# Optimization experiments

Hardware: AMD Instinct MI355X
Metric: run time of the kernel (lower is better)

Reference implementation:

```python
import jax, jax.numpy as jnp
import numpy as np

N_FFT = 256
WINDOW_OUT = 64
N_BINS = N_FFT // 2 + 1  # 129


def _irfft_matrices(n_fft, window_out):
    n = n_fft // 2 + 1
    m_real = np.fft.irfft(np.eye(n), n=n_fft)          # [n, n_fft]
    m_imag = np.fft.irfft(1j * np.eye(n), n=n_fft)     # [n, n_fft]
    m_real = m_real[:, -window_out:]                   # truncate to last window_out samples
    m_imag = m_imag[:, -window_out:]
    return (jnp.asarray(m_real, dtype=jnp.float32), jnp.asarray(m_imag, dtype=jnp.float32))


def setup_inputs() -> dict:
    key = jax.random.key(0)
    k1, k2 = jax.random.split(key)
    re = jax.random.normal(k1, (64, 4000, N_BINS), dtype=jnp.float32)
    im = jax.random.normal(k2, (64, 4000, N_BINS), dtype=jnp.float32)
    m_real, m_imag = _irfft_matrices(N_FFT, WINDOW_OUT)
    return {"re": re, "im": im, "m_real": m_real, "m_imag": m_imag}


def reference(re, im, m_real, m_imag):
    # Dense IRFFT: out = re @ M_real + im @ M_imag, fused add of the two matmul outputs.
    # re, im: [B, T, n_bins]; m_real, m_imag: [n_bins, window_out] -> out: [B, T, window_out]
    return jnp.einsum('btn,no->bto', re, m_real) + jnp.einsum('btn,no->bto', im, m_imag)
```

## Files before the change

kernel.cpp:

```cpp
#include <hip/hip_runtime.h>
#include <hip/hip_bf16.h>

typedef __bf16 bf8 __attribute__((ext_vector_type(8)));
typedef float f32x4 __attribute__((ext_vector_type(4)));

#define NBINS 129
#define ROWS_IT 16
#define ITERS 16
#define MATB 8192
#define TAILB 512
#define BUFB (2 * MATB + TAILB)

__device__ __forceinline__ void gload_lds16(const float* src, char* ldsdst) {
    __builtin_amdgcn_global_load_lds(
        (const __attribute__((address_space(1))) void*)src,
        (__attribute__((address_space(3))) void*)ldsdst, 16, 0, 0);
}

__global__ __launch_bounds__(256, 3)
void irfft_mm(const float* __restrict__ re,
              const float* __restrict__ im,
              const float* __restrict__ mr,
              const float* __restrict__ mi,
              float* __restrict__ out)
{
    __shared__ __align__(16) char lds[3][BUFB];

    const int tid  = threadIdx.x;
    const int lane = tid & 63;
    const int w    = tid >> 6;
    const int r16  = lane & 15;
    const int q    = lane >> 4;
    const int rk   = r16 & 7;

    const long blockrow = (long)blockIdx.x * (ROWS_IT * ITERS);

    const int    smat  = w >> 1;
    const int    srow0 = (w & 1) * 8;
    const float* ssrc  = smat ? im : re;
    const int    lrow  = lane >> 5;
    const int    p     = lane & 31;

    #define STAGE(bn, rbn)                                                        \
        {                                                                         \
            char* _b = (bn);                                                      \
            const long _r = (rbn);                                                \
            _Pragma("unroll")                                                     \
            for (int i = 0; i < 4; ++i) {                                         \
                const int trow = srow0 + 2 * i + lrow;                            \
                const int g    = p ^ (trow & 7);   \
                gload_lds16(ssrc + (_r + trow) * (long)NBINS + g * 4,             \
                            _b + smat * MATB + (srow0 + 2 * i) * 512 + lane * 16);\
            }                                                                     \
            if (lane < 8)      \
                gload_lds16(ssrc + (_r + srow0 + lane) * (long)NBINS + 128,       \
                            _b + 2 * MATB + smat * 256 + (srow0 + lane) * 16);    \
        }

    STAGE(lds[0], blockrow);
    STAGE(lds[1], blockrow + ROWS_IT);

    bf8 afr[2][4];
    #pragma unroll
    for (int m = 0; m < 2; ++m) {
        const float* M = m ? mi : mr;
        #pragma unroll
        for (int t = 0; t < 4; ++t) {
            bf8 a;
            #pragma unroll
            for (int j = 0; j < 8; ++j)
                a[j] = (__bf16)M[(t * 32 + q * 8 + j) * 64 + w * 16 + r16];
            afr[m][t] = a;
        }
    }
    const f32x4 mt0 = *(const f32x4*)(mr + 128 * 64 + w * 16 + q * 4);
    const f32x4 mt1 = *(const f32x4*)(mi + 128 * 64 + w * 16 + q * 4);

    #pragma unroll
    for (int it = 0; it < ITERS; ++it) {
        char* bufc = lds[it % 3];
        const long rowbase = blockrow + it * ROWS_IT;

        __builtin_amdgcn_sched_barrier(0);
        if (it < ITERS - 1) asm volatile("s_waitcnt vmcnt(5)" ::: "memory");
        else                asm volatile("s_waitcnt vmcnt(0)" ::: "memory");
        __builtin_amdgcn_s_barrier();
        __builtin_amdgcn_sched_barrier(0);

        if (it + 2 < ITERS)
            STAGE(lds[(it + 2) % 3], rowbase + 2 * ROWS_IT);

        f32x4 acc = {0.0f, 0.0f, 0.0f, 0.0f};
        #pragma unroll
        for (int m = 0; m < 2; ++m) {
            const char* mb = bufc + m * MATB + r16 * 512;
            #pragma unroll
            for (int t = 0; t < 4; ++t) {
                const int j0 = t * 8 + q * 2;
                const f32x4 lo = *(const f32x4*)(mb + ((j0)     ^ rk) * 16);
                const f32x4 hi = *(const f32x4*)(mb + ((j0 + 1) ^ rk) * 16);
                bf8 bfr;
                #pragma unroll
                for (int jj = 0; jj < 4; ++jj) {
                    bfr[jj]     = (__bf16)lo[jj];
                    bfr[4 + jj] = (__bf16)hi[jj];
                }
                acc = __builtin_amdgcn_mfma_f32_16x16x32_bf16(afr[m][t], bfr, acc, 0, 0, 0);
            }
            const float xt = *(const float*)(bufc + 2 * MATB + m * 256 + r16 * 16);
            const f32x4 mt = m ? mt1 : mt0;
            #pragma unroll
            for (int jj = 0; jj < 4; ++jj) acc[jj] += xt * mt[jj];
        }

        *(f32x4*)(out + (rowbase + r16) * 64 + w * 16 + q * 4) = acc;
    }
    #undef STAGE
}

extern "C" void kernel_launch(void* const* d_in, const int* in_sizes, int n_in,
                              void* d_out, int out_size, void* d_ws, size_t ws_size,
                              hipStream_t stream)
{
    const float* re = (const float*)d_in[0];
    const float* im = (const float*)d_in[1];
    const float* mr = (const float*)d_in[2];
    const float* mi = (const float*)d_in[3];
    float* out = (float*)d_out;

    const long rows = (long)in_sizes[0] / NBINS;
    const int grid = (int)(rows / (ROWS_IT * ITERS));
    irfft_mm<<<grid, 256, 0, stream>>>(re, im, mr, mi, out);
}
```

Before: 68.02 us.

## Use persistent fixed grid with balanced tile distribution across blocks

Replaces the launch of one block per 256 rows with a fixed grid of 768 blocks. Each block takes a contiguous, evenly balanced range of 16-row tiles, and the pipelined loop now runs for a runtime trip count. This amortizes the per-block setup (loading the M fragments, priming the pipeline) over more tiles and evens out the tail wave across CUs. In exchange the main loop is no longer fully unrolled and uses runtime buffer indexing. The old code also silently dropped any rows left over when the row count was not a multiple of 256.

```diff
diff --git a/kernel.cpp b/kernel.cpp
--- a/kernel.cpp
+++ b/kernel.cpp
@@ -5,11 +5,11 @@
 typedef float f32x4 __attribute__((ext_vector_type(4)));
 
 #define NBINS 129
-#define ROWS_IT 16
-#define ITERS 16
+#define TROWS 16
 #define MATB 8192
 #define TAILB 512
 #define BUFB (2 * MATB + TAILB)
+#define GRID 768
 
 __device__ __forceinline__ void gload_lds16(const float* src, char* ldsdst) {
     __builtin_amdgcn_global_load_lds(
@@ -22,7 +22,8 @@
               const float* __restrict__ im,
               const float* __restrict__ mr,
               const float* __restrict__ mi,
-              float* __restrict__ out)
+              float* __restrict__ out,
+              int ntiles)
 {
     __shared__ __align__(16) char lds[3][BUFB];
 
@@ -33,7 +34,11 @@
     const int q    = lane >> 4;
     const int rk   = r16 & 7;
 
-    const long blockrow = (long)blockIdx.x * (ROWS_IT * ITERS);
+    const int qt  = ntiles / GRID;
+    const int rt  = ntiles % GRID;
+    const int bid = blockIdx.x;
+    const int nit = qt + (bid < rt ? 1 : 0);
+    const long t0 = (long)bid * qt + (bid < rt ? bid : rt);
 
     const int    smat  = w >> 1;
     const int    srow0 = (w & 1) * 8;
@@ -57,8 +62,8 @@
                             _b + 2 * MATB + smat * 256 + (srow0 + lane) * 16);    \
         }
 
-    STAGE(lds[0], blockrow);
-    STAGE(lds[1], blockrow + ROWS_IT);
+    STAGE(lds[0], t0 * TROWS);
+    STAGE(lds[1], (t0 + 1) * TROWS);
 
     bf8 afr[2][4];
     #pragma unroll
@@ -76,19 +81,21 @@
     const f32x4 mt0 = *(const f32x4*)(mr + 128 * 64 + w * 16 + q * 4);
     const f32x4 mt1 = *(const f32x4*)(mi + 128 * 64 + w * 16 + q * 4);
 
-    #pragma unroll
-    for (int it = 0; it < ITERS; ++it) {
-        char* bufc = lds[it % 3];
-        const long rowbase = blockrow + it * ROWS_IT;
+    int bi = 0;
+    for (int i = 0; i < nit; ++i) {
+        char* bufc = lds[bi];
+        const long rowbase = (t0 + i) * TROWS;
 
         __builtin_amdgcn_sched_barrier(0);
-        if (it < ITERS - 1) asm volatile("s_waitcnt vmcnt(5)" ::: "memory");
-        else                asm volatile("s_waitcnt vmcnt(0)" ::: "memory");
+        if (i + 1 < nit) asm volatile("s_waitcnt vmcnt(5)" ::: "memory");
+        else             asm volatile("s_waitcnt vmcnt(0)" ::: "memory");
         __builtin_amdgcn_s_barrier();
         __builtin_amdgcn_sched_barrier(0);
 
-        if (it + 2 < ITERS)
-            STAGE(lds[(it + 2) % 3], rowbase + 2 * ROWS_IT);
+        if (i + 2 < nit) {
+            int bi2 = bi + 2; if (bi2 >= 3) bi2 -= 3;
+            STAGE(lds[bi2], (t0 + i + 2) * TROWS);
+        }
 
         f32x4 acc = {0.0f, 0.0f, 0.0f, 0.0f};
         #pragma unroll
@@ -114,6 +121,8 @@
         }
 
         *(f32x4*)(out + (rowbase + r16) * 64 + w * 16 + q * 4) = acc;
+
+        bi = (bi == 2) ? 0 : bi + 1;
     }
     #undef STAGE
 }
@@ -128,7 +137,7 @@
     const float* mi = (const float*)d_in[3];
     float* out = (float*)d_out;
 
-    const long rows = (long)in_sizes[0] / NBINS;
-    const int grid = (int)(rows / (ROWS_IT * ITERS));
-    irfft_mm<<<grid, 256, 0, stream>>>(re, im, mr, mi, out);
+    const long rows   = (long)in_sizes[0] / NBINS;
+    const int  ntiles = (int)(rows / TROWS);
+    irfft_mm<<<GRID, 256, 0, stream>>>(re, im, mr, mi, out, ntiles);
 }
```

Result: no change. 69.14 us (+1.6%).
